# Performance work log

Hardware: AMD Instinct MI355X
Metric: run time of the kernel (lower is better)

The kernel has to match this reference:

```python
import jax, jax.numpy as jnp
import numpy as np

NIN, NOUT = 256, 64

def setup_inputs() -> dict:
    key = jax.random.key(0)
    k1, k2, k3, k4 = jax.random.split(key, 4)
    B, T = 4, 4096
    y = jax.random.normal(k1, (B, T, NIN), dtype=jnp.float32)
    # torch Linear(nin, nout).weight has shape [nout, nin]; store as [nin, nout]
    s = 1.0 / np.sqrt(NIN)
    Wq = jax.random.uniform(k2, (NIN, NOUT), jnp.float32, -s, s)
    Wk = jax.random.uniform(k3, (NIN, NOUT), jnp.float32, -s, s)
    Wv = jax.random.uniform(k4, (NIN, NOUT), jnp.float32, -s, s)
    return {"y": y, "Wq": Wq, "Wk": Wk, "Wv": Wv}

def reference(y, Wq, Wk, Wv):
    T = y.shape[1]
    que = y @ Wq  # [B,T,NOUT]
    key = y @ Wk
    val = y @ Wv
    att = jnp.einsum('bqd,bkd->bqk', que, key)  # [B,T,T]
    causal = jnp.tril(jnp.ones((T, T), dtype=bool))  # True = keep
    att = jnp.where(causal, att, -jnp.inf)
    att = jax.nn.softmax(att / jnp.sqrt(jnp.float32(NOUT)), axis=-1)
    return jnp.einsum('bqk,bkd->bqd', att, val)
```

## Files before the change

### kernel.cpp

```cpp
#include <hip/hip_runtime.h>
#include <hip/hip_bf16.h>

#define TLEN 4096
#define NINP 256
#define DD   64

#define QSCALE 0.18033688011112042f

typedef __attribute__((ext_vector_type(8))) short bf16x8;
typedef __attribute__((ext_vector_type(4))) float f32x4;

union U8 { bf16x8 v; uint u[4]; };

__device__ inline ushort bfu(float x) {
    union { float f; uint u; } a; a.f = x;
    uint r = a.u + 0x7fffu + ((a.u >> 16) & 1u);
    return (ushort)(r >> 16);
}
__device__ inline bf16x8 ld16(const ushort* p) {
    return *(const bf16x8*)p;
}
__device__ inline bf16x8 ld8x2(const ushort* p) {
    U8 u;
    uint2 a = *(const uint2*)p;
    uint2 b = *(const uint2*)(p + 4);
    u.u[0] = a.x; u.u[1] = a.y; u.u[2] = b.x; u.u[3] = b.y;
    return u.v;
}

__global__ __launch_bounds__(256) void prep_wt(
    const float* __restrict__ Wq, const float* __restrict__ Wk,
    const float* __restrict__ Wv, ushort* __restrict__ WT)
{
    __shared__ ushort lt[256 * 66];
    const int t = threadIdx.x;
    const int m = blockIdx.x;
    const float* W = (m == 0) ? Wq : ((m == 1) ? Wk : Wv);
    const float scale = (m == 0) ? QSCALE : 1.0f;

    #pragma unroll
    for (int j = 0; j < 16; ++j) {
        int i4 = t + 256 * j;
        float4 v = *(const float4*)&W[i4 * 4];
        int k = i4 >> 4, d = (i4 * 4) & 63;
        uint p0 = bfu(v.x * scale) | (uint(bfu(v.y * scale)) << 16);
        uint p1 = bfu(v.z * scale) | (uint(bfu(v.w * scale)) << 16);
        *(uint*)&lt[k * 66 + d]     = p0;
        *(uint*)&lt[k * 66 + d + 2] = p1;
    }
    __syncthreads();
    #pragma unroll
    for (int j = 0; j < 64; ++j) {
        int o = t + 256 * j;
        int d = o >> 8, k = o & 255;
        WT[m * 16384 + o] = lt[k * 66 + d];
    }
}

__global__ __launch_bounds__(256, 1) void qkv_kernel(
    const float* __restrict__ y, const ushort* __restrict__ WT,
    ushort* __restrict__ Qh, ushort* __restrict__ Kh, ushort* __restrict__ VhT)
{
    __shared__ ushort Wl[64 * 260];
    __shared__ ushort tb[64 * 68];

    const int t = threadIdx.x;
    const int w = t >> 6, lane = t & 63;
    const int quad = lane >> 4, l15 = lane & 15;
    const int rowbase = blockIdx.x * 64;
    const int myrow = rowbase + w * 16 + l15;

    bf16x8 afrag[8];
    const float* yrow = y + (size_t)myrow * NINP;
    #pragma unroll
    for (int s = 0; s < 8; ++s) {
        float4 lo = *(const float4*)&yrow[s * 32 + quad * 8];
        float4 hi = *(const float4*)&yrow[s * 32 + quad * 8 + 4];
        U8 u;
        u.u[0] = bfu(lo.x) | (uint(bfu(lo.y)) << 16);
        u.u[1] = bfu(lo.z) | (uint(bfu(lo.w)) << 16);
        u.u[2] = bfu(hi.x) | (uint(bfu(hi.y)) << 16);
        u.u[3] = bfu(hi.z) | (uint(bfu(hi.w)) << 16);
        afrag[s] = u.v;
    }

    f32x4 acc[3][4];
    #pragma unroll
    for (int m = 0; m < 3; ++m)
        #pragma unroll
        for (int nt = 0; nt < 4; ++nt)
            acc[m][nt] = f32x4{0.f, 0.f, 0.f, 0.f};

    for (int m = 0; m < 3; ++m) {
        __syncthreads();
        {
            int n = t >> 2, seg = t & 3;
            const ushort* src = WT + m * 16384 + n * 256 + seg * 64;
            ushort* dst = &Wl[n * 260 + seg * 64];
            #pragma unroll
            for (int j = 0; j < 16; ++j)
                ((uint2*)dst)[j] = ((const uint2*)src)[j];
        }
        __syncthreads();
        #pragma unroll
        for (int s = 0; s < 8; ++s)
            #pragma unroll
            for (int nt = 0; nt < 4; ++nt) {
                bf16x8 bfrag = ld8x2(&Wl[(nt * 16 + l15) * 260 + s * 32 + quad * 8]);
                acc[m][nt] = __builtin_amdgcn_mfma_f32_16x16x32_bf16(
                    afrag[s], bfrag, acc[m][nt], 0, 0, 0);
            }
    }

    for (int m = 0; m < 2; ++m) {
        __syncthreads();
        #pragma unroll
        for (int nt = 0; nt < 4; ++nt)
            #pragma unroll
            for (int r = 0; r < 4; ++r)
                tb[(w * 16 + quad * 4 + r) * 68 + nt * 16 + l15] = bfu(acc[m][nt][r]);
        __syncthreads();
        int row = t >> 2, seg = t & 3;
        ushort* gd = (m == 0 ? Qh : Kh) + (size_t)(rowbase + row) * DD + seg * 16;
        const ushort* sp = &tb[row * 68 + seg * 16];
        #pragma unroll
        for (int j = 0; j < 4; ++j) ((uint2*)gd)[j] = ((const uint2*)sp)[j];
    }

    __syncthreads();
    #pragma unroll
    for (int nt = 0; nt < 4; ++nt)
        #pragma unroll
        for (int r = 0; r < 4; r += 2) {
            int d = nt * 16 + l15;
            int tt = w * 16 + quad * 4 + r;
            uint pk = bfu(acc[2][nt][r]) | (uint(bfu(acc[2][nt][r + 1])) << 16);
            *(uint*)&tb[d * 68 + tt] = pk;
        }
    __syncthreads();
    {
        int d = t >> 2, seg = t & 3;
        int bb = blockIdx.x >> 6;
        int trow = (blockIdx.x & 63) * 64 + seg * 16;
        ushort* gv = VhT + ((size_t)bb * DD + d) * TLEN + trow;
        const ushort* sp = &tb[d * 68 + seg * 16];
        #pragma unroll
        for (int j = 0; j < 4; ++j) ((uint2*)gv)[j] = ((const uint2*)sp)[j];
    }
}

__global__ __launch_bounds__(256, 1) void attn_kernel(
    const ushort* __restrict__ Qh, const ushort* __restrict__ Kh,
    const ushort* __restrict__ VhT, float* __restrict__ out)
{
    __shared__ ushort Pb[4][32 * 68];
    __shared__ float  Ob[4][2048];
    __shared__ float  lb[4][32];

    const int t = threadIdx.x;
    const int w = t >> 6, lane = t & 63;
    const int quad = lane >> 4, l15 = lane & 15;
    const int b = blockIdx.x >> 6;
    const int pr = blockIdx.x & 63;

    const ushort* Qb = Qh + (size_t)b * TLEN * DD;
    const ushort* Kb = Kh + (size_t)b * TLEN * DD;
    const ushort* Vb = VhT + (size_t)b * DD * TLEN;
    float* outb = out + (size_t)b * TLEN * DD;

    for (int half = 0; half < 2; ++half) {
        const int tile = (half == 0) ? pr : (127 - pr);
        const int seg  = (half == 0) ? w : (3 - w);
        const int qb   = tile * 32;
        const int nc   = (tile + 2) >> 1;
        const int cps  = (nc + 3) >> 2;
        const int clo  = seg * cps;
        const int chi  = (nc < clo + cps) ? nc : (clo + cps);

        f32x4 o_acc[2][4];
        #pragma unroll
        for (int qt = 0; qt < 2; ++qt)
            #pragma unroll
            for (int nt = 0; nt < 4; ++nt)
                o_acc[qt][nt] = f32x4{0.f, 0.f, 0.f, 0.f};
        float l_acc[2] = {0.f, 0.f};

        if (clo < chi) {
            bf16x8 qf[2][2];
            #pragma unroll
            for (int qt = 0; qt < 2; ++qt)
                #pragma unroll
                for (int s = 0; s < 2; ++s)
                    qf[qt][s] = ld16(Qb + (size_t)(qb + qt * 16 + l15) * DD + s * 32 + quad * 8);

            bf16x8 kf[4][2];
            {
                int c0 = clo * 64;
                #pragma unroll
                for (int kt = 0; kt < 4; ++kt)
                    #pragma unroll
                    for (int s = 0; s < 2; ++s)
                        kf[kt][s] = ld16(Kb + (size_t)(c0 + kt * 16 + l15) * DD + s * 32 + quad * 8);
            }

            for (int ci = clo; ci < chi; ++ci) {
                const int c0 = ci * 64;
                bf16x8 vf[4][2];
                #pragma unroll
                for (int nt = 0; nt < 4; ++nt)
                    #pragma unroll
                    for (int s = 0; s < 2; ++s)
                        vf[nt][s] = ld16(Vb + (size_t)(nt * 16 + l15) * TLEN + c0 + s * 32 + quad * 8);

                f32x4 st[2][4];
                #pragma unroll
                for (int qt = 0; qt < 2; ++qt)
                    #pragma unroll
                    for (int kt = 0; kt < 4; ++kt)
                        st[qt][kt] = f32x4{0.f, 0.f, 0.f, 0.f};
                #pragma unroll
                for (int s = 0; s < 2; ++s)
                    #pragma unroll
                    for (int qt = 0; qt < 2; ++qt)
                        #pragma unroll
                        for (int kt = 0; kt < 4; ++kt)
                            st[qt][kt] = __builtin_amdgcn_mfma_f32_16x16x32_bf16(
                                kf[kt][s], qf[qt][s], st[qt][kt], 0, 0, 0);

                if (ci + 1 < chi) {
                    int c1 = c0 + 64;
                    #pragma unroll
                    for (int kt = 0; kt < 4; ++kt)
                        #pragma unroll
                        for (int s = 0; s < 2; ++s)
                            kf[kt][s] = ld16(Kb + (size_t)(c1 + kt * 16 + l15) * DD + s * 32 + quad * 8);
                }

                #pragma unroll
                for (int qt = 0; qt < 2; ++qt) {
                    const int q = qb + qt * 16 + l15;
                    #pragma unroll
                    for (int kt = 0; kt < 4; ++kt) {
                        const int kbase = c0 + kt * 16 + quad * 4;
                        float p[4];
                        #pragma unroll
                        for (int r = 0; r < 4; ++r) {
                            float e = exp2f(st[qt][kt][r]);
                            p[r] = (kbase + r <= q) ? e : 0.f;
                            l_acc[qt] += p[r];
                        }
                        ushort* pw = &Pb[w][(qt * 16 + l15) * 68 + kt * 16 + quad * 4];
                        *(uint*)&pw[0] = bfu(p[0]) | (uint(bfu(p[1])) << 16);
                        *(uint*)&pw[2] = bfu(p[2]) | (uint(bfu(p[3])) << 16);
                    }
                }

                #pragma unroll
                for (int qt = 0; qt < 2; ++qt) {
                    const ushort* pr_ = &Pb[w][(qt * 16 + l15) * 68];
                    bf16x8 ap0 = ld8x2(pr_ + quad * 8);
                    bf16x8 ap1 = ld8x2(pr_ + 32 + quad * 8);
                    #pragma unroll
                    for (int nt = 0; nt < 4; ++nt) {
                        o_acc[qt][nt] = __builtin_amdgcn_mfma_f32_16x16x32_bf16(
                            ap0, vf[nt][0], o_acc[qt][nt], 0, 0, 0);
                        o_acc[qt][nt] = __builtin_amdgcn_mfma_f32_16x16x32_bf16(
                            ap1, vf[nt][1], o_acc[qt][nt], 0, 0, 0);
                    }
                }
            }

            #pragma unroll
            for (int qt = 0; qt < 2; ++qt) {
                l_acc[qt] += __shfl_xor(l_acc[qt], 16, 64);
                l_acc[qt] += __shfl_xor(l_acc[qt], 32, 64);
            }
        }

        #pragma unroll
        for (int qt = 0; qt < 2; ++qt) {
            #pragma unroll
            for (int nt = 0; nt < 4; ++nt)
                #pragma unroll
                for (int r = 0; r < 4; ++r)
                    Ob[w][(qt * 16 + quad * 4 + r) * 64 + nt * 16 + l15] = o_acc[qt][nt][r];
            if (quad == 0) lb[w][qt * 16 + l15] = l_acc[qt];
        }
        __syncthreads();

        #pragma unroll
        for (int e = 0; e < 8; ++e) {
            int idx = t + 256 * e;
            int q = idx >> 6;
            float s = Ob[0][idx] + Ob[1][idx] + Ob[2][idx] + Ob[3][idx];
            float ls = lb[0][q] + lb[1][q] + lb[2][q] + lb[3][q];
            outb[(size_t)(qb + q) * DD + (idx & 63)] = s * __builtin_amdgcn_rcpf(ls);
        }
        __syncthreads();
    }
}

extern "C" void kernel_launch(void* const* d_in, const int* in_sizes, int n_in,
                              void* d_out, int out_size, void* d_ws, size_t ws_size,
                              hipStream_t stream) {
    const float* y  = (const float*)d_in[0];
    const float* Wq = (const float*)d_in[1];
    const float* Wk = (const float*)d_in[2];
    const float* Wv = (const float*)d_in[3];
    float* outp = (float*)d_out;

    const int rows = in_sizes[0] / NINP;
    const int nb = rows / TLEN;

    ushort* WT  = (ushort*)d_ws;
    ushort* Qh  = WT + 3 * 16384;
    ushort* Kh  = Qh + (size_t)rows * DD;
    ushort* VhT = Kh + (size_t)rows * DD;

    prep_wt<<<3, 256, 0, stream>>>(Wq, Wk, Wv, WT);
    qkv_kernel<<<rows / 64, 256, 0, stream>>>(y, WT, Qh, Kh, VhT);
    attn_kernel<<<nb * 64, 256, 0, stream>>>(Qh, Kh, VhT, outp);
}
```

Before: 114.2 us.

## Keep P in registers for PV MFMA, split attention tiles, widen QKV blocks

The attention kernel now computes O transposed with 16x16x16 bf16 MFMAs, so the softmax probabilities stay in registers instead of going through LDS. Each block handles one query tile (heaviest first) instead of a pair, with occupancy 2, and an unmasked fast path skips the causal compare on fully-visible chunks. The QKV kernel uses 512 threads, loads all three weight matrices into LDS once, and splits output columns across wave pairs. Other changes are vectorized transpose writes in prep_wt and s_setprio around MFMA blocks. The trade-offs are more LDS in QKV and the risk that the uint2 V loads and smaller MFMAs cost more than they save.

```diff
diff --git a/kernel.cpp b/kernel.cpp
--- a/kernel.cpp
+++ b/kernel.cpp
@@ -8,15 +8,21 @@
 #define QSCALE 0.18033688011112042f
 
 typedef __attribute__((ext_vector_type(8))) short bf16x8;
+typedef __attribute__((ext_vector_type(4))) short bf16x4;
 typedef __attribute__((ext_vector_type(4))) float f32x4;
 
 union U8 { bf16x8 v; uint u[4]; };
+union U4 { bf16x4 v; uint u[2]; };
 
 __device__ inline ushort bfu(float x) {
     union { float f; uint u; } a; a.f = x;
     uint r = a.u + 0x7fffu + ((a.u >> 16) & 1u);
     return (ushort)(r >> 16);
 }
+__device__ inline uint pk2(float lo, float hi) {
+    return (uint)bfu(lo) | ((uint)bfu(hi) << 16);
+}
+
 __device__ inline bf16x8 ld16(const ushort* p) {
     return *(const bf16x8*)p;
 }
@@ -43,32 +49,49 @@
         int i4 = t + 256 * j;
         float4 v = *(const float4*)&W[i4 * 4];
         int k = i4 >> 4, d = (i4 * 4) & 63;
-        uint p0 = bfu(v.x * scale) | (uint(bfu(v.y * scale)) << 16);
-        uint p1 = bfu(v.z * scale) | (uint(bfu(v.w * scale)) << 16);
-        *(uint*)&lt[k * 66 + d]     = p0;
-        *(uint*)&lt[k * 66 + d + 2] = p1;
-    }
-    __syncthreads();
-    #pragma unroll
-    for (int j = 0; j < 64; ++j) {
-        int o = t + 256 * j;
-        int d = o >> 8, k = o & 255;
-        WT[m * 16384 + o] = lt[k * 66 + d];
-    }
-}
-
-__global__ __launch_bounds__(256, 1) void qkv_kernel(
+        *(uint*)&lt[k * 66 + d]     = pk2(v.x * scale, v.y * scale);
+        *(uint*)&lt[k * 66 + d + 2] = pk2(v.z * scale, v.w * scale);
+    }
+    __syncthreads();
+    #pragma unroll
+    for (int j = 0; j < 32; ++j) {
+        int o2 = t + 256 * j;
+        int d = o2 >> 7, k = (o2 & 127) * 2;
+        uint pk = (uint)lt[k * 66 + d] | ((uint)lt[(k + 1) * 66 + d] << 16);
+        *(uint*)&WT[m * 16384 + d * 256 + k] = pk;
+    }
+}
+
+__global__ __launch_bounds__(512, 1) void qkv_kernel(
     const float* __restrict__ y, const ushort* __restrict__ WT,
     ushort* __restrict__ Qh, ushort* __restrict__ Kh, ushort* __restrict__ VhT)
 {
-    __shared__ ushort Wl[64 * 260];
+    __shared__ ushort Wl[3 * 64 * 268];
     __shared__ ushort tb[64 * 68];
 
     const int t = threadIdx.x;
     const int w = t >> 6, lane = t & 63;
     const int quad = lane >> 4, l15 = lane & 15;
+    const int rowgrp = w >> 1;
+    const int nth = w & 1;
     const int rowbase = blockIdx.x * 64;
-    const int myrow = rowbase + w * 16 + l15;
+    const int myrow = rowbase + rowgrp * 16 + l15;
+
+    {
+        int id = t;
+        #pragma unroll
+        for (int rnd = 0; rnd < 2; ++rnd, id += 512) {
+            if (id < 768) {
+                int m = id >> 8, rem = id & 255;
+                int n = rem >> 2, seg = rem & 3;
+                const ushort* src = WT + m * 16384 + n * 256 + seg * 64;
+                ushort* dst = &Wl[m * 17152 + n * 268 + seg * 64];
+                #pragma unroll
+                for (int j = 0; j < 16; ++j)
+                    ((uint2*)dst)[j] = ((const uint2*)src)[j];
+            }
+        }
+    }
 
     bf16x8 afrag[8];
     const float* yrow = y + (size_t)myrow * NINP;
@@ -77,226 +100,241 @@
         float4 lo = *(const float4*)&yrow[s * 32 + quad * 8];
         float4 hi = *(const float4*)&yrow[s * 32 + quad * 8 + 4];
         U8 u;
-        u.u[0] = bfu(lo.x) | (uint(bfu(lo.y)) << 16);
-        u.u[1] = bfu(lo.z) | (uint(bfu(lo.w)) << 16);
-        u.u[2] = bfu(hi.x) | (uint(bfu(hi.y)) << 16);
-        u.u[3] = bfu(hi.z) | (uint(bfu(hi.w)) << 16);
+        u.u[0] = pk2(lo.x, lo.y);
+        u.u[1] = pk2(lo.z, lo.w);
+        u.u[2] = pk2(hi.x, hi.y);
+        u.u[3] = pk2(hi.z, hi.w);
         afrag[s] = u.v;
     }
 
-    f32x4 acc[3][4];
+    __syncthreads();
+
+    f32x4 acc[3][2];
     #pragma unroll
     for (int m = 0; m < 3; ++m)
         #pragma unroll
-        for (int nt = 0; nt < 4; ++nt)
-            acc[m][nt] = f32x4{0.f, 0.f, 0.f, 0.f};
-
-    for (int m = 0; m < 3; ++m) {
+        for (int n = 0; n < 2; ++n)
+            acc[m][n] = f32x4{0.f, 0.f, 0.f, 0.f};
+
+    #pragma unroll
+    for (int m = 0; m < 3; ++m)
+        #pragma unroll
+        for (int s = 0; s < 8; ++s)
+            #pragma unroll
+            for (int n = 0; n < 2; ++n) {
+                int nt = nth * 2 + n;
+                bf16x8 bfrag = ld8x2(&Wl[m * 17152 + (nt * 16 + l15) * 268 + s * 32 + quad * 8]);
+                acc[m][n] = __builtin_amdgcn_mfma_f32_16x16x32_bf16(
+                    afrag[s], bfrag, acc[m][n], 0, 0, 0);
+            }
+
+    #pragma unroll
+    for (int m = 0; m < 2; ++m) {
+        __syncthreads();
+        #pragma unroll
+        for (int n = 0; n < 2; ++n) {
+            int nt = nth * 2 + n;
+            #pragma unroll
+            for (int r = 0; r < 4; ++r)
+                tb[(rowgrp * 16 + quad * 4 + r) * 68 + nt * 16 + l15] = bfu(acc[m][n][r]);
+        }
         __syncthreads();
         {
-            int n = t >> 2, seg = t & 3;
-            const ushort* src = WT + m * 16384 + n * 256 + seg * 64;
-            ushort* dst = &Wl[n * 260 + seg * 64];
-            #pragma unroll
-            for (int j = 0; j < 16; ++j)
-                ((uint2*)dst)[j] = ((const uint2*)src)[j];
-        }
-        __syncthreads();
-        #pragma unroll
-        for (int s = 0; s < 8; ++s)
-            #pragma unroll
-            for (int nt = 0; nt < 4; ++nt) {
-                bf16x8 bfrag = ld8x2(&Wl[(nt * 16 + l15) * 260 + s * 32 + quad * 8]);
-                acc[m][nt] = __builtin_amdgcn_mfma_f32_16x16x32_bf16(
-                    afrag[s], bfrag, acc[m][nt], 0, 0, 0);
-            }
-    }
-
-    for (int m = 0; m < 2; ++m) {
-        __syncthreads();
-        #pragma unroll
-        for (int nt = 0; nt < 4; ++nt)
-            #pragma unroll
-            for (int r = 0; r < 4; ++r)
-                tb[(w * 16 + quad * 4 + r) * 68 + nt * 16 + l15] = bfu(acc[m][nt][r]);
-        __syncthreads();
-        int row = t >> 2, seg = t & 3;
-        ushort* gd = (m == 0 ? Qh : Kh) + (size_t)(rowbase + row) * DD + seg * 16;
-        const ushort* sp = &tb[row * 68 + seg * 16];
-        #pragma unroll
-        for (int j = 0; j < 4; ++j) ((uint2*)gd)[j] = ((const uint2*)sp)[j];
-    }
-
-    __syncthreads();
-    #pragma unroll
-    for (int nt = 0; nt < 4; ++nt)
+            int row = t >> 3, seg = t & 7;
+            ushort* gd = (m == 0 ? Qh : Kh) + (size_t)(rowbase + row) * DD + seg * 8;
+            const ushort* sp = &tb[row * 68 + seg * 8];
+            ((uint2*)gd)[0] = ((const uint2*)sp)[0];
+            ((uint2*)gd)[1] = ((const uint2*)sp)[1];
+        }
+    }
+
+    __syncthreads();
+    #pragma unroll
+    for (int n = 0; n < 2; ++n) {
+        int nt = nth * 2 + n;
+        int d = nt * 16 + l15;
         #pragma unroll
         for (int r = 0; r < 4; r += 2) {
-            int d = nt * 16 + l15;
-            int tt = w * 16 + quad * 4 + r;
-            uint pk = bfu(acc[2][nt][r]) | (uint(bfu(acc[2][nt][r + 1])) << 16);
-            *(uint*)&tb[d * 68 + tt] = pk;
-        }
+            int tt = rowgrp * 16 + quad * 4 + r;
+            *(uint*)&tb[d * 68 + tt] = pk2(acc[2][n][r], acc[2][n][r + 1]);
+        }
+    }
     __syncthreads();
     {
-        int d = t >> 2, seg = t & 3;
+        int d = t >> 3, seg = t & 7;
         int bb = blockIdx.x >> 6;
-        int trow = (blockIdx.x & 63) * 64 + seg * 16;
-        ushort* gv = VhT + ((size_t)bb * DD + d) * TLEN + trow;
-        const ushort* sp = &tb[d * 68 + seg * 16];
-        #pragma unroll
-        for (int j = 0; j < 4; ++j) ((uint2*)gv)[j] = ((const uint2*)sp)[j];
-    }
-}
-
-__global__ __launch_bounds__(256, 1) void attn_kernel(
+        int tcol = (blockIdx.x & 63) * 64 + seg * 8;
+        ushort* gv = VhT + ((size_t)bb * DD + d) * TLEN + tcol;
+        const ushort* sp = &tb[d * 68 + seg * 8];
+        ((uint2*)gv)[0] = ((const uint2*)sp)[0];
+        ((uint2*)gv)[1] = ((const uint2*)sp)[1];
+    }
+}
+
+__global__ __launch_bounds__(256, 2) void attn_kernel(
     const ushort* __restrict__ Qh, const ushort* __restrict__ Kh,
-    const ushort* __restrict__ VhT, float* __restrict__ out)
+    const ushort* __restrict__ VhT, float* __restrict__ out, const int nb)
 {
-    __shared__ ushort Pb[4][32 * 68];
-    __shared__ float  Ob[4][2048];
-    __shared__ float  lb[4][32];
+    __shared__ float Ob[4][32 * 68];
+    __shared__ float lb[4][32];
 
     const int t = threadIdx.x;
     const int w = t >> 6, lane = t & 63;
     const int quad = lane >> 4, l15 = lane & 15;
-    const int b = blockIdx.x >> 6;
-    const int pr = blockIdx.x & 63;
+    const int b = blockIdx.x % nb;
+    const int tile = 127 - blockIdx.x / nb;
+
+    const int qb = tile * 32;
+    const int nc = (tile + 2) >> 1;
+    const int cps = (nc + 3) >> 2;
+    const int clo = w * cps;
+    const int chi = (nc < clo + cps) ? nc : (clo + cps);
 
     const ushort* Qb = Qh + (size_t)b * TLEN * DD;
     const ushort* Kb = Kh + (size_t)b * TLEN * DD;
     const ushort* Vb = VhT + (size_t)b * DD * TLEN;
-    float* outb = out + (size_t)b * TLEN * DD;
-
-    for (int half = 0; half < 2; ++half) {
-        const int tile = (half == 0) ? pr : (127 - pr);
-        const int seg  = (half == 0) ? w : (3 - w);
-        const int qb   = tile * 32;
-        const int nc   = (tile + 2) >> 1;
-        const int cps  = (nc + 3) >> 2;
-        const int clo  = seg * cps;
-        const int chi  = (nc < clo + cps) ? nc : (clo + cps);
-
-        f32x4 o_acc[2][4];
+
+    f32x4 oT[2][4];
+    #pragma unroll
+    for (int qt = 0; qt < 2; ++qt)
+        #pragma unroll
+        for (int nt = 0; nt < 4; ++nt)
+            oT[qt][nt] = f32x4{0.f, 0.f, 0.f, 0.f};
+    float l_acc[2] = {0.f, 0.f};
+
+    if (clo < chi) {
+        bf16x8 qf[2][2];
         #pragma unroll
         for (int qt = 0; qt < 2; ++qt)
             #pragma unroll
+            for (int s = 0; s < 2; ++s)
+                qf[qt][s] = ld16(Qb + (size_t)(qb + qt * 16 + l15) * DD + s * 32 + quad * 8);
+
+        const ushort* vbase[4];
+        #pragma unroll
+        for (int nt = 0; nt < 4; ++nt)
+            vbase[nt] = Vb + (size_t)(nt * 16 + l15) * TLEN + quad * 4;
+
+        bf16x8 kf[4][2];
+        {
+            int c0 = clo * 64;
+            #pragma unroll
+            for (int kt = 0; kt < 4; ++kt)
+                #pragma unroll
+                for (int s = 0; s < 2; ++s)
+                    kf[kt][s] = ld16(Kb + (size_t)(c0 + kt * 16 + l15) * DD + s * 32 + quad * 8);
+        }
+
+        for (int ci = clo; ci < chi; ++ci) {
+            const int c0 = ci * 64;
+
+            U4 vt[4][4];
+            #pragma unroll
             for (int nt = 0; nt < 4; ++nt)
-                o_acc[qt][nt] = f32x4{0.f, 0.f, 0.f, 0.f};
-        float l_acc[2] = {0.f, 0.f};
-
-        if (clo < chi) {
-            bf16x8 qf[2][2];
+                #pragma unroll
+                for (int kt = 0; kt < 4; ++kt) {
+                    uint2 vv = *(const uint2*)(vbase[nt] + c0 + kt * 16);
+                    vt[nt][kt].u[0] = vv.x; vt[nt][kt].u[1] = vv.y;
+                }
+
+            f32x4 st[2][4];
             #pragma unroll
             for (int qt = 0; qt < 2; ++qt)
                 #pragma unroll
-                for (int s = 0; s < 2; ++s)
-                    qf[qt][s] = ld16(Qb + (size_t)(qb + qt * 16 + l15) * DD + s * 32 + quad * 8);
-
-            bf16x8 kf[4][2];
-            {
-                int c0 = clo * 64;
-                #pragma unroll
                 for (int kt = 0; kt < 4; ++kt)
+                    st[qt][kt] = f32x4{0.f, 0.f, 0.f, 0.f};
+            __builtin_amdgcn_s_setprio(1);
+            #pragma unroll
+            for (int s = 0; s < 2; ++s)
+                #pragma unroll
+                for (int qt = 0; qt < 2; ++qt)
+                    #pragma unroll
+                    for (int kt = 0; kt < 4; ++kt)
+                        st[qt][kt] = __builtin_amdgcn_mfma_f32_16x16x32_bf16(
+                            kf[kt][s], qf[qt][s], st[qt][kt], 0, 0, 0);
+            __builtin_amdgcn_s_setprio(0);
+
+            if (ci + 1 < chi) {
+                int c1 = c0 + 64;
+                #pragma unroll
+                for (int kt = 0; kt < 4; ++kt)
                     #pragma unroll
                     for (int s = 0; s < 2; ++s)
-                        kf[kt][s] = ld16(Kb + (size_t)(c0 + kt * 16 + l15) * DD + s * 32 + quad * 8);
+                        kf[kt][s] = ld16(Kb + (size_t)(c1 + kt * 16 + l15) * DD + s * 32 + quad * 8);
             }
 
-            for (int ci = clo; ci < chi; ++ci) {
-                const int c0 = ci * 64;
-                bf16x8 vf[4][2];
-                #pragma unroll
-                for (int nt = 0; nt < 4; ++nt)
-                    #pragma unroll
-                    for (int s = 0; s < 2; ++s)
-                        vf[nt][s] = ld16(Vb + (size_t)(nt * 16 + l15) * TLEN + c0 + s * 32 + quad * 8);
-
-                f32x4 st[2][4];
+            U4 pa[2][4];
+            if (c0 + 63 <= qb) {
                 #pragma unroll
                 for (int qt = 0; qt < 2; ++qt)
                     #pragma unroll
-                    for (int kt = 0; kt < 4; ++kt)
-                        st[qt][kt] = f32x4{0.f, 0.f, 0.f, 0.f};
-                #pragma unroll
-                for (int s = 0; s < 2; ++s)
-                    #pragma unroll
-                    for (int qt = 0; qt < 2; ++qt)
-                        #pragma unroll
-                        for (int kt = 0; kt < 4; ++kt)
-                            st[qt][kt] = __builtin_amdgcn_mfma_f32_16x16x32_bf16(
-                                kf[kt][s], qf[qt][s], st[qt][kt], 0, 0, 0);
-
-                if (ci + 1 < chi) {
-                    int c1 = c0 + 64;
-                    #pragma unroll
-                    for (int kt = 0; kt < 4; ++kt)
-                        #pragma unroll
-                        for (int s = 0; s < 2; ++s)
-                            kf[kt][s] = ld16(Kb + (size_t)(c1 + kt * 16 + l15) * DD + s * 32 + quad * 8);
-                }
-
+                    for (int kt = 0; kt < 4; ++kt) {
+                        float p0 = exp2f(st[qt][kt][0]);
+                        float p1 = exp2f(st[qt][kt][1]);
+                        float p2 = exp2f(st[qt][kt][2]);
+                        float p3 = exp2f(st[qt][kt][3]);
+                        l_acc[qt] += (p0 + p1) + (p2 + p3);
+                        pa[qt][kt].u[0] = pk2(p0, p1);
+                        pa[qt][kt].u[1] = pk2(p2, p3);
+                    }
+            } else {
                 #pragma unroll
                 for (int qt = 0; qt < 2; ++qt) {
                     const int q = qb + qt * 16 + l15;
                     #pragma unroll
                     for (int kt = 0; kt < 4; ++kt) {
-                        const int kbase = c0 + kt * 16 + quad * 4;
+                        const int kb0 = c0 + kt * 16 + quad * 4;
                         float p[4];
                         #pragma unroll
                         for (int r = 0; r < 4; ++r) {
                             float e = exp2f(st[qt][kt][r]);
-                            p[r] = (kbase + r <= q) ? e : 0.f;
+                            p[r] = (kb0 + r <= q) ? e : 0.f;
                             l_acc[qt] += p[r];
                         }
-                        ushort* pw = &Pb[w][(qt * 16 + l15) * 68 + kt * 16 + quad * 4];
-                        *(uint*)&pw[0] = bfu(p[0]) | (uint(bfu(p[1])) << 16);
-                        *(uint*)&pw[2] = bfu(p[2]) | (uint(bfu(p[3])) << 16);
-                    }
-                }
-
-                #pragma unroll
-                for (int qt = 0; qt < 2; ++qt) {
-                    const ushort* pr_ = &Pb[w][(qt * 16 + l15) * 68];
-                    bf16x8 ap0 = ld8x2(pr_ + quad * 8);
-                    bf16x8 ap1 = ld8x2(pr_ + 32 + quad * 8);
-                    #pragma unroll
-                    for (int nt = 0; nt < 4; ++nt) {
-                        o_acc[qt][nt] = __builtin_amdgcn_mfma_f32_16x16x32_bf16(
-                            ap0, vf[nt][0], o_acc[qt][nt], 0, 0, 0);
-                        o_acc[qt][nt] = __builtin_amdgcn_mfma_f32_16x16x32_bf16(
-                            ap1, vf[nt][1], o_acc[qt][nt], 0, 0, 0);
+                        pa[qt][kt].u[0] = pk2(p[0], p[1]);
+                        pa[qt][kt].u[1] = pk2(p[2], p[3]);
                     }
                 }
             }
 
-            #pragma unroll
-            for (int qt = 0; qt < 2; ++qt) {
-                l_acc[qt] += __shfl_xor(l_acc[qt], 16, 64);
-                l_acc[qt] += __shfl_xor(l_acc[qt], 32, 64);
-            }
+            __builtin_amdgcn_s_setprio(1);
+            #pragma unroll
+            for (int qt = 0; qt < 2; ++qt)
+                #pragma unroll
+                for (int nt = 0; nt < 4; ++nt)
+                    #pragma unroll
+                    for (int kt = 0; kt < 4; ++kt)
+                        oT[qt][nt] = __builtin_amdgcn_mfma_f32_16x16x16bf16_1k(
+                            vt[nt][kt].v, pa[qt][kt].v, oT[qt][nt], 0, 0, 0);
+            __builtin_amdgcn_s_setprio(0);
         }
 
         #pragma unroll
         for (int qt = 0; qt < 2; ++qt) {
-            #pragma unroll
-            for (int nt = 0; nt < 4; ++nt)
-                #pragma unroll
-                for (int r = 0; r < 4; ++r)
-                    Ob[w][(qt * 16 + quad * 4 + r) * 64 + nt * 16 + l15] = o_acc[qt][nt][r];
-            if (quad == 0) lb[w][qt * 16 + l15] = l_acc[qt];
-        }
-        __syncthreads();
-
-        #pragma unroll
-        for (int e = 0; e < 8; ++e) {
-            int idx = t + 256 * e;
-            int q = idx >> 6;
-            float s = Ob[0][idx] + Ob[1][idx] + Ob[2][idx] + Ob[3][idx];
-            float ls = lb[0][q] + lb[1][q] + lb[2][q] + lb[3][q];
-            outb[(size_t)(qb + q) * DD + (idx & 63)] = s * __builtin_amdgcn_rcpf(ls);
-        }
-        __syncthreads();
+            l_acc[qt] += __shfl_xor(l_acc[qt], 16, 64);
+            l_acc[qt] += __shfl_xor(l_acc[qt], 32, 64);
+        }
+    }
+
+    #pragma unroll
+    for (int qt = 0; qt < 2; ++qt) {
+        #pragma unroll
+        for (int nt = 0; nt < 4; ++nt)
+            #pragma unroll
+            for (int r = 0; r < 4; ++r)
+                Ob[w][(qt * 16 + l15) * 68 + nt * 16 + quad * 4 + r] = oT[qt][nt][r];
+        if (quad == 0) lb[w][qt * 16 + l15] = l_acc[qt];
+    }
+    __syncthreads();
+
+    float* outb = out + (size_t)b * TLEN * DD;
+    #pragma unroll
+    for (int e = 0; e < 8; ++e) {
+        int idx = t + 256 * e;
+        int q = idx >> 6, d = idx & 63;
+        float s = Ob[0][q * 68 + d] + Ob[1][q * 68 + d] + Ob[2][q * 68 + d] + Ob[3][q * 68 + d];
+        float ls = lb[0][q] + lb[1][q] + lb[2][q] + lb[3][q];
+        outb[(size_t)(qb + q) * DD + d] = s * __builtin_amdgcn_rcpf(ls);
     }
 }
 
@@ -318,6 +356,6 @@
     ushort* VhT = Kh + (size_t)rows * DD;
 
     prep_wt<<<3, 256, 0, stream>>>(Wq, Wk, Wv, WT);
-    qkv_kernel<<<rows / 64, 256, 0, stream>>>(y, WT, Qh, Kh, VhT);
-    attn_kernel<<<nb * 64, 256, 0, stream>>>(Qh, Kh, VhT, outp);
-}
+    qkv_kernel<<<rows / 64, 512, 0, stream>>>(y, WT, Qh, Kh, VhT);
+    attn_kernel<<<nb * 128, 256, 0, stream>>>(Qh, Kh, VhT, outp, nb);
+}
```

Measured after the change: 144.3 us. 1.26x slower.
